# Performance work log

Measured on AMD Instinct MI355X. Metric: run time of the kernel, lower is better.

Reference implementation:

```python
import jax, jax.numpy as jnp
import numpy as np
import math

B, H, W, D = 4, 64, 64, 256
N, K, V = 8, 32, 32


def setup_inputs() -> dict:
    key = jax.random.key(0)
    ks = jax.random.split(key, 7)
    blob = jax.random.normal(ks[0], (B, H, W, D), dtype=jnp.float32)
    # 1x1 conv kernels == dense [D, out] matrices; glorot-ish scale
    s = 1.0 / math.sqrt(D)
    wq = jax.random.normal(ks[1], (D, N * K), dtype=jnp.float32) * s
    wk = jax.random.normal(ks[2], (D, N * K), dtype=jnp.float32) * s
    wv = jax.random.normal(ks[3], (D, N * V), dtype=jnp.float32) * s
    bq = jnp.zeros((N * K,), jnp.float32)
    bk = jnp.zeros((N * K,), jnp.float32)
    bv = jnp.zeros((N * V,), jnp.float32)
    return {"blob": blob, "wq": wq, "bq": bq, "wk": wk, "bk": bk, "wv": wv, "bv": bv}


def _maxpool2x2(x):
    # MaxPool2D with pool_size=strides=(2,2), VALID padding, NHWC
    return jax.lax.reduce_window(
        x, -jnp.inf, jax.lax.max,
        window_dimensions=(1, 2, 2, 1), window_strides=(1, 2, 2, 1), padding="VALID")


def reference(blob, wq, bq, wk, bk, wv, bv):
    H2, W2 = H // 2, W // 2
    # pooled query path
    q = _maxpool2x2(blob)                                   # [B,H2,W2,D]
    q = (q @ wq + bq).reshape(B, H2, W2, N, K)              # [B,H2,W2,N,K]
    q = q * (1.0 / math.sqrt(float(K)))
    # key/value paths (1x1 conv == per-pixel matmul); swish on value
    k = (blob @ wk + bk).reshape(B, H * W, N, K)            # [B,HW,N,K]
    v = jax.nn.swish(blob @ wv + bv).reshape(B, H * W, N, V)  # [B,HW,N,V]
    # cross-attention: contract K, outer product of pooled grid with full grid
    scores = jnp.einsum("bhwnk,bink->bhwin", q, k)          # [B,H2,W2,HW,N]
    attn = jax.nn.softmax(scores, axis=3)                   # softmax over HW
    out = jnp.einsum("bhwin,binv->bhwnv", attn, v)          # [B,H2,W2,N,V]
    return out.reshape(B, H2, W2, N * V)
```

## Files before the change

kernel.cpp:

```cpp
#include <hip/hip_runtime.h>


typedef _Float16 f16x8 __attribute__((ext_vector_type(8)));
typedef _Float16 f16x4 __attribute__((ext_vector_type(4)));
typedef float    f32x4 __attribute__((ext_vector_type(4)));

#define F16(x) static_cast<_Float16>(x)

#if __has_builtin(__builtin_amdgcn_exp2f)
#define EXP2(x) __builtin_amdgcn_exp2f(x)
#else
#define EXP2(x) exp2f(x)
#endif

__device__ __forceinline__ void gl_lds16(const void* g, void* l) {
    __builtin_amdgcn_global_load_lds(
        (const __attribute__((address_space(1))) unsigned int*)g,
        (__attribute__((address_space(3))) unsigned int*)l, 16, 0, 0);
}

__global__ __launch_bounds__(256) void prep_kernel(
    const float* __restrict__ wq, const float* __restrict__ wk,
    const float* __restrict__ wv, _Float16* __restrict__ wt) {
    __shared__ float t[32][33];
    const int blk = blockIdx.x;
    const int mat = blk >> 6;
    const int tile = blk & 63;
    const int d0 = (tile >> 3) * 32, o0 = (tile & 7) * 32;
    const float* w = (mat == 0) ? wq : (mat == 1 ? wk : wv);
    const int tx = threadIdx.x & 31, ty = threadIdx.x >> 5;
#pragma unroll
    for (int i = 0; i < 4; ++i)
        t[ty + i * 8][tx] = w[(d0 + ty + i * 8) * 256 + o0 + tx];
    __syncthreads();
#pragma unroll
    for (int i = 0; i < 4; ++i)
        wt[(mat << 16) + (o0 + ty + i * 8) * 256 + d0 + tx] = (_Float16)t[tx][ty + i * 8];
}

__global__ __launch_bounds__(256) void proj_kernel(
    const float* __restrict__ blob, const _Float16* __restrict__ wt,
    const float* __restrict__ bq, const float* __restrict__ bk, const float* __restrict__ bv,
    _Float16* __restrict__ qo, _Float16* __restrict__ ko, _Float16* __restrict__ vo) {
    __shared__ __align__(16) char atile[2][4096];

    const int tid = threadIdx.x;
    const int lane = tid & 63, wid = tid >> 6;
    const int quad = lane >> 4, l16 = lane & 15;
    int jb = blockIdx.x;
    int job, rowblk;
    if (jb < 64)       { job = 0; rowblk = jb; }
    else if (jb < 320) { job = 1; rowblk = jb - 64; }
    else               { job = 2; rowblk = jb - 320; }
    const int rowbase = rowblk * 64;
    const int colbase = wid * 64;
    const _Float16* wmat = wt + ((size_t)job << 16);
    const float* bias = (job == 0) ? bq : (job == 1 ? bk : bv);

    const int srow = tid >> 2, sc8 = tid & 3;
    const int sslot = srow * 4 + ((sc8 + (srow >> 2)) & 3);
    const float* aptr;
    if (job == 0) {
        const int grow = rowbase + srow;
        const int bb = grow >> 10, y = (grow >> 5) & 31, x = grow & 31;
        aptr = blob + (((bb * 64 + 2 * y) * 64) + 2 * x) * 256 + sc8 * 8;
    } else {
        aptr = blob + (size_t)(rowbase + srow) * 256 + sc8 * 8;
    }

    const _Float16* wptr[4];
#pragma unroll
    for (int nt = 0; nt < 4; ++nt)
        wptr[nt] = wmat + (size_t)(colbase + nt * 16 + l16) * 256 + quad * 8;

    const int aread = l16 * 64 + ((quad + (l16 >> 2)) & 3) * 16;

    f32x4 acc[4][4];
#pragma unroll
    for (int mc = 0; mc < 4; ++mc)
#pragma unroll
        for (int nt = 0; nt < 4; ++nt) acc[mc][nt] = (f32x4){0.f, 0.f, 0.f, 0.f};

    f16x8 wf[3][4];
    float4 ar[2][2];

    auto A_LOAD = [&](int t, float4* dst) {
        const float* p = aptr + t * 32;
        if (job == 0) {
            float4 a0 = *(const float4*)(p);
            float4 a1 = *(const float4*)(p + 4);
            float4 b0 = *(const float4*)(p + 256);
            float4 b1 = *(const float4*)(p + 260);
            float4 c0 = *(const float4*)(p + 16384);
            float4 c1 = *(const float4*)(p + 16388);
            float4 d0 = *(const float4*)(p + 16640);
            float4 d1 = *(const float4*)(p + 16644);
            dst[0].x = fmaxf(fmaxf(a0.x, b0.x), fmaxf(c0.x, d0.x));
            dst[0].y = fmaxf(fmaxf(a0.y, b0.y), fmaxf(c0.y, d0.y));
            dst[0].z = fmaxf(fmaxf(a0.z, b0.z), fmaxf(c0.z, d0.z));
            dst[0].w = fmaxf(fmaxf(a0.w, b0.w), fmaxf(c0.w, d0.w));
            dst[1].x = fmaxf(fmaxf(a1.x, b1.x), fmaxf(c1.x, d1.x));
            dst[1].y = fmaxf(fmaxf(a1.y, b1.y), fmaxf(c1.y, d1.y));
            dst[1].z = fmaxf(fmaxf(a1.z, b1.z), fmaxf(c1.z, d1.z));
            dst[1].w = fmaxf(fmaxf(a1.w, b1.w), fmaxf(c1.w, d1.w));
        } else {
            dst[0] = *(const float4*)(p);
            dst[1] = *(const float4*)(p + 4);
        }
    };
    auto A_WRITE = [&](int buf, const float4* src) {
        auto c0 = __builtin_amdgcn_cvt_pkrtz(src[0].x, src[0].y);
        auto c1 = __builtin_amdgcn_cvt_pkrtz(src[0].z, src[0].w);
        auto c2 = __builtin_amdgcn_cvt_pkrtz(src[1].x, src[1].y);
        auto c3 = __builtin_amdgcn_cvt_pkrtz(src[1].z, src[1].w);
        f16x8 v = {F16(c0[0]), F16(c0[1]), F16(c1[0]), F16(c1[1]),
                   F16(c2[0]), F16(c2[1]), F16(c3[0]), F16(c3[1])};
        *(f16x8*)(atile[buf] + sslot * 16) = v;
    };
    auto W_LOAD = [&](int t, f16x8* dst) {
#pragma unroll
        for (int nt = 0; nt < 4; ++nt) dst[nt] = *(const f16x8*)(wptr[nt] + t * 32);
    };

    W_LOAD(0, wf[0]);
    W_LOAD(1, wf[1]);
    A_LOAD(0, ar[0]);
    A_WRITE(0, ar[0]);
    A_LOAD(1, ar[1]);
    asm volatile("s_waitcnt lgkmcnt(0)\n\ts_barrier" ::: "memory");

#pragma unroll
    for (int s = 0; s < 8; ++s) {
        if (s < 6) W_LOAD(s + 2, wf[(s + 2) % 3]);
        f16x8 af[4];
#pragma unroll
        for (int mc = 0; mc < 4; ++mc)
            af[mc] = *(const f16x8*)(atile[s & 1] + mc * 1024 + aread);
#pragma unroll
        for (int mc = 0; mc < 4; ++mc)
#pragma unroll
            for (int nt = 0; nt < 4; ++nt)
                acc[mc][nt] = __builtin_amdgcn_mfma_f32_16x16x32_f16(
                    af[mc], wf[s % 3][nt], acc[mc][nt], 0, 0, 0);
        if (s < 7) A_WRITE((s + 1) & 1, ar[(s + 1) & 1]);
        if (s < 6) A_LOAD(s + 2, ar[s & 1]);
        if (s < 7) asm volatile("s_waitcnt lgkmcnt(0)\n\ts_barrier" ::: "memory");
    }

#pragma unroll
    for (int nt = 0; nt < 4; ++nt) {
        const int o = colbase + nt * 16 + l16;
        const float bs = bias[o];
        const int nh = o >> 5, kk = o & 31;
#pragma unroll
        for (int mc = 0; mc < 4; ++mc) {
            if (job == 0) {
#pragma unroll
                for (int r = 0; r < 4; ++r) {
                    const int grow = rowbase + mc * 16 + quad * 4 + r;
                    const float x = (acc[mc][nt][r] + bs) * 0.25503508f;
                    const int bb = grow >> 10, mm = grow & 1023;
                    qo[(((bb * 8 + nh) * 1024 + mm) << 5) + kk] = (_Float16)x;
                }
            } else if (job == 1) {
#pragma unroll
                for (int r = 0; r < 4; ++r) {
                    const int grow = rowbase + mc * 16 + quad * 4 + r;
                    const float x = acc[mc][nt][r] + bs;
                    const int bb = grow >> 12, ii = grow & 4095;
                    ko[(((bb * 8 + nh) * 4096 + ii) << 5) + kk] = (_Float16)x;
                }
            } else {
                const int grow0 = rowbase + mc * 16 + quad * 4;
                const int bb = grow0 >> 12, i0 = grow0 & 4095;
                f16x4 pv;
#pragma unroll
                for (int r = 0; r < 4; ++r) {
                    float x = acc[mc][nt][r] + bs;
                    const float sg = 1.0f / (1.0f + __expf(-x));
                    pv[r] = (_Float16)(x * sg);
                }
                *(f16x4*)(vo + (size_t)(bb * 8 + nh) * 131072 + (i0 >> 4) * 512
                             + ((kk & 15) + quad * 16) * 8 + (kk >> 4) * 4) = pv;
            }
        }
    }
}

__global__ __launch_bounds__(512, 4) void attn_kernel(
    const _Float16* __restrict__ qb,
    const _Float16* __restrict__ kb,
    const _Float16* __restrict__ vf,
    float* __restrict__ out) {
    __shared__ __align__(16) char pool[49152];

    const int tid = threadIdx.x;
    const int lane = tid & 63, wid = tid >> 6;
    const int quad = lane >> 4, l16 = lane & 15;
    const int bn = blockIdx.x & 31, mt = blockIdx.x >> 5;
    const int b = bn >> 3, n = bn & 7;
    const int m0 = mt * 64;
    const int rg = wid & 3, kc = wid >> 2;

    const _Float16* gsrc[2];
    int ldsoff[2];
#pragma unroll
    for (int jj = 0; jj < 2; ++jj) {
        const int j = wid + jj * 8;
        const int kcj = j >> 3, sub = j & 7;
        if (sub < 4) {
            gsrc[jj] = kb + ((size_t)bn << 17)
                     + (size_t)(kcj * 2048 + sub * 16 + (lane & 15)) * 32 + (lane >> 4) * 8;
            ldsoff[jj] = kcj * 24576 + sub * 1024;
        } else {
            gsrc[jj] = vf + ((size_t)bn << 17)
                     + (size_t)(kcj * 128 + (sub - 4)) * 512 + lane * 8;
            ldsoff[jj] = kcj * 24576 + 4096 + (sub - 4) * 1024;
        }
    }

    const f16x8 qf = *(const f16x8*)(qb + (((size_t)(bn << 10) + m0 + rg * 16 + l16) << 5) + quad * 8);

    const int rbase = kc * 24576 + lane * 16;

#pragma unroll
    for (int p = 0; p < 2; ++p)
#pragma unroll
        for (int jj = 0; jj < 2; ++jj) {
            gl_lds16(gsrc[jj], pool + ldsoff[jj] + p * 8192);
            gsrc[jj] += 2048;
        }
    asm volatile("s_waitcnt vmcnt(2)\n\ts_barrier" ::: "memory");

    f32x4 acc0 = (f32x4){0.f, 0.f, 0.f, 0.f};
    f32x4 acc1 = acc0;
    float ps0 = 0.f;

    for (int s = 0; s < 32; ++s) {
        if (s < 30) {
            const int nb = ((s + 2) % 3) * 8192;
#pragma unroll
            for (int jj = 0; jj < 2; ++jj) {
                gl_lds16(gsrc[jj], pool + ldsoff[jj] + nb);
                gsrc[jj] += 2048;
            }
        }
        const char* base = pool + rbase + (s % 3) * 8192;
#pragma unroll
        for (int tloc = 0; tloc < 4; ++tloc) {
            const f16x8 kf = *(const f16x8*)(base + tloc * 1024);
            const f16x8 vv = *(const f16x8*)(base + 4096 + tloc * 1024);
            const f16x4 va0 = {vv[0], vv[1], vv[2], vv[3]};
            const f16x4 va1 = {vv[4], vv[5], vv[6], vv[7]};

            f32x4 s0 = __builtin_amdgcn_mfma_f32_16x16x32_f16(kf, qf, (f32x4){0.f,0.f,0.f,0.f}, 0, 0, 0);
            const float p0 = EXP2(s0[0]), p1 = EXP2(s0[1]), p2 = EXP2(s0[2]), p3 = EXP2(s0[3]);
            ps0 += (p0 + p1) + (p2 + p3);
            auto e0 = __builtin_amdgcn_cvt_pkrtz(p0, p1);
            auto e1 = __builtin_amdgcn_cvt_pkrtz(p2, p3);
            const f16x4 pb = {F16(e0[0]), F16(e0[1]), F16(e1[0]), F16(e1[1])};
            acc0 = __builtin_amdgcn_mfma_f32_16x16x16f16(va0, pb, acc0, 0, 0, 0);
            acc1 = __builtin_amdgcn_mfma_f32_16x16x16f16(va1, pb, acc1, 0, 0, 0);
        }
        if (s < 30)       asm volatile("s_waitcnt vmcnt(2)\n\ts_barrier" ::: "memory");
        else if (s == 30) asm volatile("s_waitcnt vmcnt(0)\n\ts_barrier" ::: "memory");
        else              asm volatile("s_barrier" ::: "memory");
    }

    float* num = (float*)pool;
    float* den = (float*)(pool + 64 * 33 * 4);
    for (int i = tid; i < 64 * 33 + 64; i += 512) ((float*)pool)[i] = 0.f;
    __syncthreads();

    ps0 += __shfl_xor(ps0, 16); ps0 += __shfl_xor(ps0, 32);

    const int m = rg * 16 + l16;
#pragma unroll
    for (int r = 0; r < 4; ++r) {
        atomicAdd(&num[m * 33 + quad * 4 + r], acc0[r]);
        atomicAdd(&num[m * 33 + 16 + quad * 4 + r], acc1[r]);
    }
    if (quad == 0) atomicAdd(&den[m], ps0);
    __syncthreads();

    {
        const int mloc = tid >> 3, v4 = (tid & 7) * 4;
        const float inv = 1.0f / den[mloc];
        const float* nr = num + mloc * 33 + v4;
        float4 o = {nr[0] * inv, nr[1] * inv, nr[2] * inv, nr[3] * inv};
        *(float4*)(out + (((size_t)(b << 10) + m0 + mloc) << 8) + n * 32 + v4) = o;
    }
}

extern "C" void kernel_launch(void* const* d_in, const int* in_sizes, int n_in,
                              void* d_out, int out_size, void* d_ws, size_t ws_size,
                              hipStream_t stream) {
    const float* blob = (const float*)d_in[0];
    const float* wq = (const float*)d_in[1];
    const float* bq = (const float*)d_in[2];
    const float* wk = (const float*)d_in[3];
    const float* bk = (const float*)d_in[4];
    const float* wv = (const float*)d_in[5];
    const float* bv = (const float*)d_in[6];
    float* out = (float*)d_out;

    char* ws = (char*)d_ws;
    _Float16* wt = (_Float16*)(ws);
    _Float16* ko = (_Float16*)(ws + 393216);
    _Float16* vo = (_Float16*)(ws + 8781824);
    _Float16* qo = (_Float16*)(ws + 17170432);

    prep_kernel<<<192, 256, 0, stream>>>(wq, wk, wv, wt);
    proj_kernel<<<576, 256, 0, stream>>>(blob, wt, bq, bk, bv, qo, ko, vo);
    attn_kernel<<<512, 512, 0, stream>>>(qo, ko, vo, out);
}
```

Before: 134.3 us.

## Load K/V directly into registers and give each wave two query tiles

The attention kernel stops staging K/V tiles in LDS through global_load_lds with a triple buffer and per-step barriers. Instead each wave streams its own key range straight from global memory into a rotating register buffer. Each wave now handles 32 query rows (two MFMA query fragments) over 512 keys, reusing every K/V load twice. The grid doubles to 1024 blocks with launch bounds of 6 blocks per CU. This removes the LDS traffic and barrier stalls in the main loop, at the cost of more register pressure, uncoalesced-ish per-wave global loads, and reliance on cache for reuse across blocks.

```diff
diff --git a/kernel.cpp b/kernel.cpp
--- a/kernel.cpp
+++ b/kernel.cpp
@@ -12,12 +12,6 @@
 #else
 #define EXP2(x) exp2f(x)
 #endif
-
-__device__ __forceinline__ void gl_lds16(const void* g, void* l) {
-    __builtin_amdgcn_global_load_lds(
-        (const __attribute__((address_space(1))) unsigned int*)g,
-        (__attribute__((address_space(3))) unsigned int*)l, 16, 0, 0);
-}
 
 __global__ __launch_bounds__(256) void prep_kernel(
     const float* __restrict__ wq, const float* __restrict__ wk,
@@ -187,108 +181,99 @@
     }
 }
 
-__global__ __launch_bounds__(512, 4) void attn_kernel(
+__global__ __launch_bounds__(512, 6) void attn_kernel(
     const _Float16* __restrict__ qb,
     const _Float16* __restrict__ kb,
     const _Float16* __restrict__ vf,
     float* __restrict__ out) {
-    __shared__ __align__(16) char pool[49152];
+    __shared__ float pool[32 * 33 + 32];
 
     const int tid = threadIdx.x;
-    const int lane = tid & 63, wid = tid >> 6;
+    const int lane = tid & 63, kc = tid >> 6;
     const int quad = lane >> 4, l16 = lane & 15;
     const int bn = blockIdx.x & 31, mt = blockIdx.x >> 5;
     const int b = bn >> 3, n = bn & 7;
-    const int m0 = mt * 64;
-    const int rg = wid & 3, kc = wid >> 2;
-
-    const _Float16* gsrc[2];
-    int ldsoff[2];
-#pragma unroll
-    for (int jj = 0; jj < 2; ++jj) {
-        const int j = wid + jj * 8;
-        const int kcj = j >> 3, sub = j & 7;
-        if (sub < 4) {
-            gsrc[jj] = kb + ((size_t)bn << 17)
-                     + (size_t)(kcj * 2048 + sub * 16 + (lane & 15)) * 32 + (lane >> 4) * 8;
-            ldsoff[jj] = kcj * 24576 + sub * 1024;
-        } else {
-            gsrc[jj] = vf + ((size_t)bn << 17)
-                     + (size_t)(kcj * 128 + (sub - 4)) * 512 + lane * 8;
-            ldsoff[jj] = kcj * 24576 + 4096 + (sub - 4) * 1024;
+    const int m0 = mt * 32;
+    const int key0 = kc << 9;
+
+    f16x8 qf[2];
+#pragma unroll
+    for (int mc = 0; mc < 2; ++mc)
+        qf[mc] = *(const f16x8*)(qb + (((size_t)(bn << 10) + m0 + mc * 16 + l16) << 5) + quad * 8);
+
+    const size_t bnoff = (size_t)bn << 17;
+    const _Float16* kp = kb + bnoff + (size_t)(key0 + l16) * 32 + quad * 8;
+    const _Float16* vp = vf + bnoff + (size_t)(key0 >> 4) * 512 + lane * 8;
+
+    f16x8 kr[4], vr[4];
+    kr[0] = *(const f16x8*)(kp);       vr[0] = *(const f16x8*)(vp);
+    kr[1] = *(const f16x8*)(kp + 512); vr[1] = *(const f16x8*)(vp + 512);
+    kp += 1024; vp += 1024;
+
+    f32x4 acc[2][2];
+    acc[0][0] = (f32x4){0.f, 0.f, 0.f, 0.f}; acc[0][1] = acc[0][0];
+    acc[1][0] = acc[0][0];                    acc[1][1] = acc[0][0];
+    float ps0 = 0.f, ps1 = 0.f;
+
+#pragma unroll 4
+    for (int s = 0; s < 32; ++s) {
+        const f16x8 kf = kr[s & 3];
+        const f16x8 vv = vr[s & 3];
+        if (s < 30) {
+            kr[(s + 2) & 3] = *(const f16x8*)(kp); kp += 512;
+            vr[(s + 2) & 3] = *(const f16x8*)(vp); vp += 512;
         }
-    }
-
-    const f16x8 qf = *(const f16x8*)(qb + (((size_t)(bn << 10) + m0 + rg * 16 + l16) << 5) + quad * 8);
-
-    const int rbase = kc * 24576 + lane * 16;
-
-#pragma unroll
-    for (int p = 0; p < 2; ++p)
-#pragma unroll
-        for (int jj = 0; jj < 2; ++jj) {
-            gl_lds16(gsrc[jj], pool + ldsoff[jj] + p * 8192);
-            gsrc[jj] += 2048;
-        }
-    asm volatile("s_waitcnt vmcnt(2)\n\ts_barrier" ::: "memory");
-
-    f32x4 acc0 = (f32x4){0.f, 0.f, 0.f, 0.f};
-    f32x4 acc1 = acc0;
-    float ps0 = 0.f;
-
-    for (int s = 0; s < 32; ++s) {
-        if (s < 30) {
-            const int nb = ((s + 2) % 3) * 8192;
-#pragma unroll
-            for (int jj = 0; jj < 2; ++jj) {
-                gl_lds16(gsrc[jj], pool + ldsoff[jj] + nb);
-                gsrc[jj] += 2048;
-            }
-        }
-        const char* base = pool + rbase + (s % 3) * 8192;
-#pragma unroll
-        for (int tloc = 0; tloc < 4; ++tloc) {
-            const f16x8 kf = *(const f16x8*)(base + tloc * 1024);
-            const f16x8 vv = *(const f16x8*)(base + 4096 + tloc * 1024);
-            const f16x4 va0 = {vv[0], vv[1], vv[2], vv[3]};
-            const f16x4 va1 = {vv[4], vv[5], vv[6], vv[7]};
-
-            f32x4 s0 = __builtin_amdgcn_mfma_f32_16x16x32_f16(kf, qf, (f32x4){0.f,0.f,0.f,0.f}, 0, 0, 0);
-            const float p0 = EXP2(s0[0]), p1 = EXP2(s0[1]), p2 = EXP2(s0[2]), p3 = EXP2(s0[3]);
-            ps0 += (p0 + p1) + (p2 + p3);
-            auto e0 = __builtin_amdgcn_cvt_pkrtz(p0, p1);
-            auto e1 = __builtin_amdgcn_cvt_pkrtz(p2, p3);
-            const f16x4 pb = {F16(e0[0]), F16(e0[1]), F16(e1[0]), F16(e1[1])};
-            acc0 = __builtin_amdgcn_mfma_f32_16x16x16f16(va0, pb, acc0, 0, 0, 0);
-            acc1 = __builtin_amdgcn_mfma_f32_16x16x16f16(va1, pb, acc1, 0, 0, 0);
-        }
-        if (s < 30)       asm volatile("s_waitcnt vmcnt(2)\n\ts_barrier" ::: "memory");
-        else if (s == 30) asm volatile("s_waitcnt vmcnt(0)\n\ts_barrier" ::: "memory");
-        else              asm volatile("s_barrier" ::: "memory");
-    }
-
-    float* num = (float*)pool;
-    float* den = (float*)(pool + 64 * 33 * 4);
-    for (int i = tid; i < 64 * 33 + 64; i += 512) ((float*)pool)[i] = 0.f;
+        const f16x4 va0 = {vv[0], vv[1], vv[2], vv[3]};
+        const f16x4 va1 = {vv[4], vv[5], vv[6], vv[7]};
+
+        f32x4 s0 = __builtin_amdgcn_mfma_f32_16x16x32_f16(kf, qf[0], (f32x4){0.f,0.f,0.f,0.f}, 0, 0, 0);
+        f32x4 s1 = __builtin_amdgcn_mfma_f32_16x16x32_f16(kf, qf[1], (f32x4){0.f,0.f,0.f,0.f}, 0, 0, 0);
+        const float p0 = EXP2(s0[0]), p1 = EXP2(s0[1]), p2 = EXP2(s0[2]), p3 = EXP2(s0[3]);
+        const float u0 = EXP2(s1[0]), u1 = EXP2(s1[1]), u2 = EXP2(s1[2]), u3 = EXP2(s1[3]);
+        ps0 += (p0 + p1) + (p2 + p3);
+        ps1 += (u0 + u1) + (u2 + u3);
+        auto e0 = __builtin_amdgcn_cvt_pkrtz(p0, p1);
+        auto e1 = __builtin_amdgcn_cvt_pkrtz(p2, p3);
+        auto e2 = __builtin_amdgcn_cvt_pkrtz(u0, u1);
+        auto e3 = __builtin_amdgcn_cvt_pkrtz(u2, u3);
+        const f16x4 pb0 = {F16(e0[0]), F16(e0[1]), F16(e1[0]), F16(e1[1])};
+        const f16x4 pb1 = {F16(e2[0]), F16(e2[1]), F16(e3[0]), F16(e3[1])};
+        acc[0][0] = __builtin_amdgcn_mfma_f32_16x16x16f16(va0, pb0, acc[0][0], 0, 0, 0);
+        acc[0][1] = __builtin_amdgcn_mfma_f32_16x16x16f16(va1, pb0, acc[0][1], 0, 0, 0);
+        acc[1][0] = __builtin_amdgcn_mfma_f32_16x16x16f16(va0, pb1, acc[1][0], 0, 0, 0);
+        acc[1][1] = __builtin_amdgcn_mfma_f32_16x16x16f16(va1, pb1, acc[1][1], 0, 0, 0);
+    }
+
+    float* num = pool;
+    float* den = pool + 32 * 33;
+    for (int i = tid; i < 32 * 33 + 32; i += 512) pool[i] = 0.f;
+
+    ps0 += __shfl_xor(ps0, 16); ps0 += __shfl_xor(ps0, 32);
+    ps1 += __shfl_xor(ps1, 16); ps1 += __shfl_xor(ps1, 32);
+
     __syncthreads();
 
-    ps0 += __shfl_xor(ps0, 16); ps0 += __shfl_xor(ps0, 32);
-
-    const int m = rg * 16 + l16;
-#pragma unroll
-    for (int r = 0; r < 4; ++r) {
-        atomicAdd(&num[m * 33 + quad * 4 + r], acc0[r]);
-        atomicAdd(&num[m * 33 + 16 + quad * 4 + r], acc1[r]);
-    }
-    if (quad == 0) atomicAdd(&den[m], ps0);
+#pragma unroll
+    for (int mc = 0; mc < 2; ++mc) {
+        const int m = mc * 16 + l16;
+#pragma unroll
+        for (int vc = 0; vc < 2; ++vc)
+#pragma unroll
+            for (int r = 0; r < 4; ++r)
+                atomicAdd(&num[m * 33 + vc * 16 + quad * 4 + r], acc[mc][vc][r]);
+    }
+    if (quad == 0) {
+        atomicAdd(&den[l16], ps0);
+        atomicAdd(&den[16 + l16], ps1);
+    }
     __syncthreads();
 
     {
-        const int mloc = tid >> 3, v4 = (tid & 7) * 4;
+        const int mloc = tid >> 4, v2 = (tid & 15) * 2;
         const float inv = 1.0f / den[mloc];
-        const float* nr = num + mloc * 33 + v4;
-        float4 o = {nr[0] * inv, nr[1] * inv, nr[2] * inv, nr[3] * inv};
-        *(float4*)(out + (((size_t)(b << 10) + m0 + mloc) << 8) + n * 32 + v4) = o;
+        const float* nr = num + mloc * 33 + v2;
+        float2 o = {nr[0] * inv, nr[1] * inv};
+        *(float2*)(out + (((size_t)(b << 10) + m0 + mloc) << 8) + n * 32 + v2) = o;
     }
 }
 
@@ -312,5 +297,5 @@
 
     prep_kernel<<<192, 256, 0, stream>>>(wq, wk, wv, wt);
     proj_kernel<<<576, 256, 0, stream>>>(blob, wt, bq, bk, bv, qo, ko, vo);
-    attn_kernel<<<512, 512, 0, stream>>>(qo, ko, vo, out);
+    attn_kernel<<<1024, 512, 0, stream>>>(qo, ko, vo, out);
 }
```

After: 188.2 us. 40.2% more time.

## Halve attention query tile to 32 rows, double-buffer LDS, split keys four ways

Applied to the files above, without the earlier changes.

The attention kernel now gives each block 32 query rows instead of 64, which doubles the grid to 1024 blocks. Each block's 8 waves split into 2 row groups and 4 key quarters, where before they formed 4 row groups and 2 key halves. The triple-buffered LDS pipeline becomes a double buffer with smaller stages, cutting shared memory to 32KB and letting launch bounds target 8 blocks per CU. The aim is more parallelism and occupancy. In exchange it loads K/V from global twice as often per output row and waits with a full vmcnt(0) barrier every stage, which loses prefetch depth.

```diff
diff --git a/kernel.cpp b/kernel.cpp
--- a/kernel.cpp
+++ b/kernel.cpp
@@ -187,69 +187,67 @@
     }
 }
 
-__global__ __launch_bounds__(512, 4) void attn_kernel(
+__global__ __launch_bounds__(512, 8) void attn_kernel(
     const _Float16* __restrict__ qb,
     const _Float16* __restrict__ kb,
     const _Float16* __restrict__ vf,
     float* __restrict__ out) {
-    __shared__ __align__(16) char pool[49152];
+    __shared__ __align__(16) char pool[32768];
 
     const int tid = threadIdx.x;
     const int lane = tid & 63, wid = tid >> 6;
     const int quad = lane >> 4, l16 = lane & 15;
     const int bn = blockIdx.x & 31, mt = blockIdx.x >> 5;
     const int b = bn >> 3, n = bn & 7;
-    const int m0 = mt * 64;
-    const int rg = wid & 3, kc = wid >> 2;
+    const int m0 = mt * 32;
+    const int rg = wid & 1, q = wid >> 1;
 
     const _Float16* gsrc[2];
     int ldsoff[2];
 #pragma unroll
     for (int jj = 0; jj < 2; ++jj) {
         const int j = wid + jj * 8;
-        const int kcj = j >> 3, sub = j & 7;
-        if (sub < 4) {
+        const int qj = j >> 2, sub = j & 3;
+        if (sub < 2) {
             gsrc[jj] = kb + ((size_t)bn << 17)
-                     + (size_t)(kcj * 2048 + sub * 16 + (lane & 15)) * 32 + (lane >> 4) * 8;
-            ldsoff[jj] = kcj * 24576 + sub * 1024;
+                     + (size_t)(qj * 1024 + sub * 16 + (lane & 15)) * 32 + (lane >> 4) * 8;
+            ldsoff[jj] = qj * 8192 + sub * 1024;
         } else {
             gsrc[jj] = vf + ((size_t)bn << 17)
-                     + (size_t)(kcj * 128 + (sub - 4)) * 512 + lane * 8;
-            ldsoff[jj] = kcj * 24576 + 4096 + (sub - 4) * 1024;
+                     + (size_t)(qj * 64 + (sub - 2)) * 512 + lane * 8;
+            ldsoff[jj] = qj * 8192 + 2048 + (sub - 2) * 1024;
         }
     }
 
     const f16x8 qf = *(const f16x8*)(qb + (((size_t)(bn << 10) + m0 + rg * 16 + l16) << 5) + quad * 8);
 
-    const int rbase = kc * 24576 + lane * 16;
-
-#pragma unroll
-    for (int p = 0; p < 2; ++p)
-#pragma unroll
-        for (int jj = 0; jj < 2; ++jj) {
-            gl_lds16(gsrc[jj], pool + ldsoff[jj] + p * 8192);
-            gsrc[jj] += 2048;
-        }
-    asm volatile("s_waitcnt vmcnt(2)\n\ts_barrier" ::: "memory");
+    const int rbase = q * 8192 + lane * 16;
+
+#pragma unroll
+    for (int jj = 0; jj < 2; ++jj) {
+        gl_lds16(gsrc[jj], pool + ldsoff[jj]);
+        gsrc[jj] += 1024;
+    }
+    asm volatile("s_waitcnt vmcnt(0) lgkmcnt(0)\n\ts_barrier" ::: "memory");
 
     f32x4 acc0 = (f32x4){0.f, 0.f, 0.f, 0.f};
     f32x4 acc1 = acc0;
     float ps0 = 0.f;
 
     for (int s = 0; s < 32; ++s) {
-        if (s < 30) {
-            const int nb = ((s + 2) % 3) * 8192;
+        if (s < 31) {
+            const int nb = ((s + 1) & 1) * 4096;
 #pragma unroll
             for (int jj = 0; jj < 2; ++jj) {
                 gl_lds16(gsrc[jj], pool + ldsoff[jj] + nb);
-                gsrc[jj] += 2048;
+                gsrc[jj] += 1024;
             }
         }
-        const char* base = pool + rbase + (s % 3) * 8192;
-#pragma unroll
-        for (int tloc = 0; tloc < 4; ++tloc) {
+        const char* base = pool + rbase + (s & 1) * 4096;
+#pragma unroll
+        for (int tloc = 0; tloc < 2; ++tloc) {
             const f16x8 kf = *(const f16x8*)(base + tloc * 1024);
-            const f16x8 vv = *(const f16x8*)(base + 4096 + tloc * 1024);
+            const f16x8 vv = *(const f16x8*)(base + 2048 + tloc * 1024);
             const f16x4 va0 = {vv[0], vv[1], vv[2], vv[3]};
             const f16x4 va1 = {vv[4], vv[5], vv[6], vv[7]};
 
@@ -262,14 +260,17 @@
             acc0 = __builtin_amdgcn_mfma_f32_16x16x16f16(va0, pb, acc0, 0, 0, 0);
             acc1 = __builtin_amdgcn_mfma_f32_16x16x16f16(va1, pb, acc1, 0, 0, 0);
         }
-        if (s < 30)       asm volatile("s_waitcnt vmcnt(2)\n\ts_barrier" ::: "memory");
-        else if (s == 30) asm volatile("s_waitcnt vmcnt(0)\n\ts_barrier" ::: "memory");
-        else              asm volatile("s_barrier" ::: "memory");
-    }
-
+        if (s < 31) {
+            __builtin_amdgcn_sched_barrier(0);
+            asm volatile("s_waitcnt vmcnt(0) lgkmcnt(0)\n\ts_barrier" ::: "memory");
+        }
+    }
+
+    __builtin_amdgcn_sched_barrier(0);
+    __syncthreads();
     float* num = (float*)pool;
-    float* den = (float*)(pool + 64 * 33 * 4);
-    for (int i = tid; i < 64 * 33 + 64; i += 512) ((float*)pool)[i] = 0.f;
+    float* den = (float*)(pool + 32 * 33 * 4);
+    for (int i = tid; i < 32 * 33 + 32; i += 512) ((float*)pool)[i] = 0.f;
     __syncthreads();
 
     ps0 += __shfl_xor(ps0, 16); ps0 += __shfl_xor(ps0, 32);
@@ -284,11 +285,11 @@
     __syncthreads();
 
     {
-        const int mloc = tid >> 3, v4 = (tid & 7) * 4;
+        const int mloc = tid >> 4, v2 = (tid & 15) * 2;
         const float inv = 1.0f / den[mloc];
-        const float* nr = num + mloc * 33 + v4;
-        float4 o = {nr[0] * inv, nr[1] * inv, nr[2] * inv, nr[3] * inv};
-        *(float4*)(out + (((size_t)(b << 10) + m0 + mloc) << 8) + n * 32 + v4) = o;
+        const float* nr = num + mloc * 33 + v2;
+        float2 o = {nr[0] * inv, nr[1] * inv};
+        *(float2*)(out + (((size_t)(b << 10) + m0 + mloc) << 8) + n * 32 + v2) = o;
     }
 }
 
@@ -312,5 +313,5 @@
 
     prep_kernel<<<192, 256, 0, stream>>>(wq, wk, wv, wt);
     proj_kernel<<<576, 256, 0, stream>>>(blob, wt, bq, bk, bv, qo, ko, vo);
-    attn_kernel<<<512, 512, 0, stream>>>(qo, ko, vo, out);
-}
+    attn_kernel<<<1024, 512, 0, stream>>>(qo, ko, vo, out);
+}
```

Result: slower. 146.2 us (+8.8%).
